# Kernel optimization log

Measured on AMD Instinct MI355X. Metric: run time of the kernel, lower is better.

The kernel has to match this reference:

```python
import jax, jax.numpy as jnp
import numpy as np

B, S, D, DQKV = 4, 2048, 1024, 1024

def setup_inputs() -> dict:
    key = jax.random.key(0)
    kx, kq, kk, kv = jax.random.split(key, 4)
    scale = 1.0 / np.sqrt(D)
    return {
        "x": jax.random.normal(kx, (B, S, D), dtype=jnp.float32),
        "wq": jax.random.normal(kq, (D, DQKV), dtype=jnp.float32) * scale,
        "wk": jax.random.normal(kk, (D, DQKV), dtype=jnp.float32) * scale,
        "wv": jax.random.normal(kv, (D, DQKV), dtype=jnp.float32) * scale,
    }

def reference(x, wq, wk, wv):
    # QKV projections: [B,S,D] @ [D,Dqkv] -> [B,S,Dqkv]
    q = jnp.einsum('bsd,de->bse', x, wq)
    k = jnp.einsum('bsd,de->bse', x, wk)
    v = jnp.einsum('bsd,de->bse', x, wv)
    # scores: [B,S,S], scaled by sqrt(dim_qkv)
    scores = jnp.einsum('bik,bjk->bij', q, k) / jnp.sqrt(jnp.asarray(DQKV, dtype=x.dtype))
    attn = jax.nn.softmax(scores, axis=-1)
    # output: [B,S,Dqkv]
    return jnp.einsum('bij,bjd->bid', attn, v)
```

## Files before the change

### kernel.cpp

```cpp
#include <hip/hip_runtime.h>
#include <cstdint>
#include <cstddef>

typedef __bf16 bf16;
typedef __bf16 bf16x4 __attribute__((ext_vector_type(4)));
typedef __bf16 bf16x8 __attribute__((ext_vector_type(8)));
typedef float  f32x4  __attribute__((ext_vector_type(4)));

#define BATCH 4
#define SEQ   2048
#define DIM   1024
#define LDP   2112

__device__ __forceinline__ bf16 to_bf16(float f) {
    unsigned u = __builtin_bit_cast(unsigned, f);
    u += 0x7fffu + ((u >> 16) & 1u);
    unsigned short h = (unsigned short)(u >> 16);
    return __builtin_bit_cast(bf16, h);
}

__device__ __forceinline__ void load16_lds(const bf16* g, bf16* l) {
    __builtin_amdgcn_global_load_lds(
        (__attribute__((address_space(1))) void*)(g),
        (__attribute__((address_space(3))) void*)(l),
        16, 0, 0);
}

#define BARRIER() do { asm volatile("" ::: "memory"); \
                       __builtin_amdgcn_s_barrier();  \
                       asm volatile("" ::: "memory"); } while (0)
#define LGKM0()   asm volatile("s_waitcnt lgkmcnt(0)" ::: "memory")
#define VM0()     asm volatile("s_waitcnt vmcnt(0)" ::: "memory")


__device__ __forceinline__ void stage_half(
    const bf16* __restrict__ srcRow0, int ld, int k0, bf16* dstHalfBase)
{
    const int tid  = threadIdx.x;
    const int wave = tid >> 6;
    const int lane = tid & 63;
    const int rg   = lane >> 3;
    const int scoff = ((lane & 7) ^ rg) * 8;
#pragma unroll
    for (int j = 0; j < 2; ++j) {
        const int r = wave * 16 + j * 8;
        load16_lds(srcRow0 + (size_t)(r + rg) * ld + k0 + scoff,
                   dstHalfBase + r * 64);
    }
}

__device__ __forceinline__ void gemm_big_core(
    const bf16* __restrict__ Ablk, const bf16* __restrict__ Bblk,
    int K, int lda, int ldb, bf16* As, bf16* Bs, f32x4 acc[8][4])
{
    const int tid  = threadIdx.x;
    const int lane = tid & 63;
    const int wave = tid >> 6;
    const int wr   = wave >> 2;
    const int wc   = wave & 3;
    const int r16  = lane & 15;
    const int g    = lane >> 4;
    const int r7   = r16 & 7;
    const int pk0  = ((g) ^ r7) * 8;
    const int pk1  = ((4 + g) ^ r7) * 8;
    const int arow = (wr * 128 + r16) * 64;
    const int brow = (wc * 64 + r16) * 64;
    const int NT   = K >> 6;

    stage_half(Bblk, ldb, 0, Bs);
    stage_half(Bblk + (size_t)128 * ldb, ldb, 0, Bs + 8192);
    stage_half(Ablk, lda, 0, As);
    stage_half(Ablk + (size_t)128 * lda, lda, 0, As + 8192);
    VM0();
    BARRIER();

#pragma unroll 2
    for (int t = 0; t < NT; ++t) {
        bf16* Ac = As + (t & 1) * 16384;
        bf16* Bc = Bs + (t & 1) * 16384;
        bf16* An = As + ((t + 1) & 1) * 16384;
        bf16* Bn = Bs + ((t + 1) & 1) * 16384;
        const int k1 = (t + 1) << 6;

        bf16x8 b[4][2], a[4][2], a2[4][2];
#pragma unroll
        for (int n = 0; n < 4; ++n) {
            b[n][0] = *(const bf16x8*)(Bc + brow + n * 1024 + pk0);
            b[n][1] = *(const bf16x8*)(Bc + brow + n * 1024 + pk1);
        }
#pragma unroll
        for (int m = 0; m < 4; ++m) {
            a[m][0] = *(const bf16x8*)(Ac + arow + m * 1024 + pk0);
            a[m][1] = *(const bf16x8*)(Ac + arow + m * 1024 + pk1);
        }
        if (t + 1 < NT) {
            stage_half(Bblk, ldb, k1, Bn);
            stage_half(Bblk + (size_t)128 * ldb, ldb, k1, Bn + 8192);
            stage_half(Ablk, lda, k1, An);
            stage_half(Ablk + (size_t)128 * lda, lda, k1, An + 8192);
        }
#pragma unroll
        for (int m = 0; m < 4; ++m)
#pragma unroll
            for (int n = 0; n < 4; ++n)
#pragma unroll
                for (int ks = 0; ks < 2; ++ks)
                    acc[m][n] = __builtin_amdgcn_mfma_f32_16x16x32_bf16(
                        a[m][ks], b[n][ks], acc[m][n], 0, 0, 0);
#pragma unroll
        for (int m = 0; m < 4; ++m) {
            a2[m][0] = *(const bf16x8*)(Ac + arow + 4096 + m * 1024 + pk0);
            a2[m][1] = *(const bf16x8*)(Ac + arow + 4096 + m * 1024 + pk1);
        }
#pragma unroll
        for (int m = 0; m < 4; ++m)
#pragma unroll
            for (int n = 0; n < 4; ++n)
#pragma unroll
                for (int ks = 0; ks < 2; ++ks)
                    acc[4 + m][n] = __builtin_amdgcn_mfma_f32_16x16x32_bf16(
                        a2[m][ks], b[n][ks], acc[4 + m][n], 0, 0, 0);

        LGKM0();
        if (t + 1 < NT) VM0();
        BARRIER();
    }
}

__device__ __forceinline__ void gemm_big_core_n128(
    const bf16* __restrict__ Ablk, const bf16* __restrict__ Bblk,
    int K, int lda, int ldb, bf16* As, bf16* Bs, f32x4 acc[4][4])
{
    const int tid  = threadIdx.x;
    const int lane = tid & 63;
    const int wave = tid >> 6;
    const int wr   = wave >> 1;
    const int wc   = wave & 1;
    const int r16  = lane & 15;
    const int g    = lane >> 4;
    const int r7   = r16 & 7;
    const int pk0  = ((g) ^ r7) * 8;
    const int pk1  = ((4 + g) ^ r7) * 8;
    const int arow = (wr * 64 + r16) * 64;
    const int brow = (wc * 64 + r16) * 64;
    const int NT   = K >> 6;

    stage_half(Ablk, lda, 0, As);
    stage_half(Ablk + (size_t)128 * lda, lda, 0, As + 8192);
    stage_half(Bblk, ldb, 0, Bs);
    VM0();
    BARRIER();

#pragma unroll 2
    for (int t = 0; t < NT; ++t) {
        bf16* Ac = As + (t & 1) * 16384;
        bf16* Bc = Bs + (t & 1) * 8192;
        bf16* An = As + ((t + 1) & 1) * 16384;
        bf16* Bn = Bs + ((t + 1) & 1) * 8192;
        const int k1 = (t + 1) << 6;

        bf16x8 a[4][2], b[4][2];
#pragma unroll
        for (int n = 0; n < 4; ++n) {
            b[n][0] = *(const bf16x8*)(Bc + brow + n * 1024 + pk0);
            b[n][1] = *(const bf16x8*)(Bc + brow + n * 1024 + pk1);
        }
#pragma unroll
        for (int m = 0; m < 4; ++m) {
            a[m][0] = *(const bf16x8*)(Ac + arow + m * 1024 + pk0);
            a[m][1] = *(const bf16x8*)(Ac + arow + m * 1024 + pk1);
        }
        if (t + 1 < NT) {
            stage_half(Ablk, lda, k1, An);
            stage_half(Ablk + (size_t)128 * lda, lda, k1, An + 8192);
            stage_half(Bblk, ldb, k1, Bn);
        }
#pragma unroll
        for (int m = 0; m < 4; ++m)
#pragma unroll
            for (int n = 0; n < 4; ++n)
#pragma unroll
                for (int ks = 0; ks < 2; ++ks)
                    acc[m][n] = __builtin_amdgcn_mfma_f32_16x16x32_bf16(
                        a[m][ks], b[n][ks], acc[m][n], 0, 0, 0);

        LGKM0();
        if (t + 1 < NT) VM0();
        BARRIER();
    }
}

__device__ __forceinline__ void write_c256(
    bf16* __restrict__ Cb, int ldc, const f32x4 acc[8][4])
{
    const int lane = threadIdx.x & 63;
    const int wave = threadIdx.x >> 6;
    const int wr = wave >> 2, wc = wave & 3;
    const int r16 = lane & 15, g = lane >> 4;
    const int row0 = wr * 128 + g * 4;
    const int col0 = wc * 64 + r16;
#pragma unroll
    for (int m = 0; m < 8; ++m)
#pragma unroll
        for (int n = 0; n < 4; ++n)
#pragma unroll
            for (int rr = 0; rr < 4; ++rr)
                Cb[(size_t)(row0 + m * 16 + rr) * ldc + col0 + n * 16] =
                    to_bf16(acc[m][n][rr]);
}

__device__ __forceinline__ void write_c128n(
    bf16* __restrict__ Cb, int ldc, const f32x4 acc[4][4])
{
    const int lane = threadIdx.x & 63;
    const int wave = threadIdx.x >> 6;
    const int wr = wave >> 1, wc = wave & 1;
    const int r16 = lane & 15, g = lane >> 4;
    const int row0 = wr * 64 + g * 4;
    const int col0 = wc * 64 + r16;
#pragma unroll
    for (int m = 0; m < 4; ++m)
#pragma unroll
        for (int n = 0; n < 4; ++n)
#pragma unroll
            for (int rr = 0; rr < 4; ++rr)
                Cb[(size_t)(row0 + m * 16 + rr) * ldc + col0 + n * 16] =
                    to_bf16(acc[m][n][rr]);
}

__global__ __launch_bounds__(512, 2) void proj_qk(
    const bf16* __restrict__ xb, const bf16* __restrict__ Wt,
    bf16* __restrict__ Q, bf16* __restrict__ Kb)
{
    __shared__ bf16 As[32768];
    __shared__ bf16 Bs[32768];
    f32x4 acc[8][4] = {};

    const int p = blockIdx.x;
    const int x = p & 7, s = p >> 3;
    const int my = x * 4 + (s >> 3);
    const int j  = s & 7;
    const bf16* Ab = xb + (size_t)my * 256 * DIM;
    const bf16* Bb = Wt + (size_t)((j >> 2) ? DIM * DIM : 0)
                        + (size_t)(j & 3) * 256 * DIM;
    bf16* dst = (j >> 2) ? Kb : Q;
    bf16* Cb = dst + (size_t)my * 256 * DIM + (size_t)(j & 3) * 256;

    gemm_big_core(Ab, Bb, DIM, DIM, DIM, As, Bs, acc);
    write_c256(Cb, DIM, acc);
}

__global__ __launch_bounds__(512, 2) void proj_v(
    const bf16* __restrict__ xb, const bf16* __restrict__ Wt,
    bf16* __restrict__ Vt)
{
    __shared__ bf16 As[32768];
    __shared__ bf16 Bs[16384];
    f32x4 acc[4][4] = {};

    const int p = blockIdx.x;
    const int x = p & 7, s = p >> 3;
    const int bz = x & 3;
    const int vy = s >> 3;
    const int vx = (x >> 2) * 8 + (s & 7);
    const bf16* Ab = Wt + (size_t)2 * DIM * DIM + (size_t)vy * 256 * DIM;
    const bf16* Bb = xb + (size_t)bz * SEQ * DIM + (size_t)vx * 128 * DIM;
    bf16* Cb = Vt + (size_t)bz * DIM * LDP + (size_t)vy * 256 * LDP
                  + (size_t)vx * 128;

    gemm_big_core_n128(Ab, Bb, DIM, DIM, DIM, As, Bs, acc);
    write_c128n(Cb, LDP, acc);
}

__global__ __launch_bounds__(512, 2) void gemm_scores8(
    const bf16* __restrict__ Qm, const bf16* __restrict__ Kb,
    bf16* __restrict__ P, float* __restrict__ lsum)
{
    __shared__ bf16 As[32768];
    __shared__ bf16 Bs[32768];
    f32x4 acc[8][4] = {};

    const int p = blockIdx.x;
    const int x = p & 7, s = p >> 3;
    const int bz = x & 3;
    const int by = (x >> 2) * 4 + (s >> 3);
    const int bx = s & 7;
    const bf16* Ab = Qm + (size_t)bz * SEQ * DIM + (size_t)by * 256 * DIM;
    const bf16* Bb = Kb + (size_t)bz * SEQ * DIM + (size_t)bx * 256 * DIM;
    gemm_big_core(Ab, Bb, DIM, DIM, DIM, As, Bs, acc);

    bf16* Cb  = P + (size_t)bz * SEQ * LDP;
    float* ls = lsum + (size_t)bz * SEQ;
    const int lane = threadIdx.x & 63;
    const int wave = threadIdx.x >> 6;
    const int wr = wave >> 2, wc = wave & 3;
    const int r16 = lane & 15, g = lane >> 4;
    const int rowB = by * 256 + wr * 128 + g * 4;
    const int colB = bx * 256 + wc * 64 + r16;
#pragma unroll
    for (int m = 0; m < 8; ++m)
#pragma unroll
        for (int rr = 0; rr < 4; ++rr) {
            float sum = 0.0f;
#pragma unroll
            for (int n = 0; n < 4; ++n) {
                const float e = __expf(acc[m][n][rr] * 0.03125f);
                sum += e;
                Cb[(size_t)(rowB + m * 16 + rr) * LDP + colB + n * 16] = to_bf16(e);
            }
            sum += __shfl_xor(sum, 1);
            sum += __shfl_xor(sum, 2);
            sum += __shfl_xor(sum, 4);
            sum += __shfl_xor(sum, 8);
            if (r16 == 0)
                atomicAdd(ls + rowB + m * 16 + rr, sum);
        }
}

__global__ __launch_bounds__(512, 2) void gemm_pv8(
    const bf16* __restrict__ P, const bf16* __restrict__ Vt,
    float* __restrict__ C, const float* __restrict__ lsum)
{
    __shared__ bf16 As[32768];
    __shared__ bf16 Bs[16384];
    f32x4 acc[4][4] = {};

    const int p = blockIdx.x;
    const int x = p & 7, s = p >> 3;
    const int bz = x & 3;
    const int by = (x >> 2) * 4 + (s >> 3);
    const int bx = s & 7;
    const bf16* Ab = P  + (size_t)bz * SEQ * LDP + (size_t)by * 256 * LDP;
    const bf16* Bb = Vt + (size_t)bz * DIM * LDP + (size_t)bx * 128 * LDP;
    gemm_big_core_n128(Ab, Bb, SEQ, LDP, LDP, As, Bs, acc);

    float* Cb = C + (size_t)bz * SEQ * DIM;
    const float* ls = lsum + (size_t)bz * SEQ;
    const int lane = threadIdx.x & 63;
    const int wave = threadIdx.x >> 6;
    const int wr = wave >> 1, wc = wave & 1;
    const int r16 = lane & 15, g = lane >> 4;
    const int row0 = by * 256 + wr * 64 + g * 4;
    const int col0 = bx * 128 + wc * 64 + r16;
#pragma unroll
    for (int m = 0; m < 4; ++m)
#pragma unroll
        for (int rr = 0; rr < 4; ++rr) {
            const int row = row0 + m * 16 + rr;
            const float inv = __builtin_amdgcn_rcpf(ls[row]);
#pragma unroll
            for (int n = 0; n < 4; ++n)
                Cb[(size_t)row * DIM + col0 + n * 16] = acc[m][n][rr] * inv;
        }
}

__global__ __launch_bounds__(256) void prep(
    const float* __restrict__ x,  const float* __restrict__ wq,
    const float* __restrict__ wk, const float* __restrict__ wv,
    bf16* __restrict__ xb, bf16* __restrict__ Wt, float* __restrict__ lsum)
{
    __shared__ float tile[32][33];
    const int b = blockIdx.x;
    const int tid = threadIdx.x;
    if (b < 8192) {
        const size_t i = ((size_t)b * 256 + tid) * 4;
        const float4 v = *(const float4*)(x + i);
        bf16x4 o = { to_bf16(v.x), to_bf16(v.y), to_bf16(v.z), to_bf16(v.w) };
        *(bf16x4*)(xb + i) = o;
    } else if (b < 8192 + 3072) {
        const int t   = b - 8192;
        const int sel = t >> 10;
        const int n0  = (t & 31) * 32;
        const int k0  = ((t >> 5) & 31) * 32;
        const float* w = (sel == 0) ? wq : (sel == 1) ? wk : wv;
        const int tx = tid & 31, ty = tid >> 5;
#pragma unroll
        for (int j = 0; j < 32; j += 8)
            tile[ty + j][tx] = w[(size_t)(k0 + ty + j) * 1024 + n0 + tx];
        __syncthreads();
        bf16* dst = Wt + (size_t)sel * 1024 * 1024;
#pragma unroll
        for (int j = 0; j < 32; j += 8)
            dst[(size_t)(n0 + ty + j) * 1024 + k0 + tx] = to_bf16(tile[tx][ty + j]);
    } else {
#pragma unroll
        for (int i = 0; i < 32; ++i)
            lsum[i * 256 + tid] = 0.0f;
    }
}

extern "C" void kernel_launch(void* const* d_in, const int* in_sizes, int n_in,
                              void* d_out, int out_size, void* d_ws, size_t ws_size,
                              hipStream_t stream)
{
    const float* x  = (const float*)d_in[0];
    const float* wq = (const float*)d_in[1];
    const float* wk = (const float*)d_in[2];
    const float* wv = (const float*)d_in[3];
    float* out = (float*)d_out;
    char* ws = (char*)d_ws;

    bf16*  xb   = (bf16*)(ws);
    bf16*  Wt   = (bf16*)(ws + (16u << 20));
    bf16*  Q    = (bf16*)(ws + (22u << 20));
    bf16*  Kb   = (bf16*)(ws + (38u << 20));
    bf16*  Vt   = (bf16*)(ws + (54u << 20));
    bf16*  P    = (bf16*)(ws + (72u << 20));
    float* lsum = (float*)(ws + (108u << 20));

    prep<<<dim3(8192 + 3072 + 1), dim3(256), 0, stream>>>(
        x, wq, wk, wv, xb, Wt, lsum);

    proj_qk<<<dim3(256), dim3(512), 0, stream>>>(xb, Wt, Q, Kb);
    proj_v<<<dim3(256), dim3(512), 0, stream>>>(xb, Wt, Vt);

    gemm_scores8<<<dim3(256), dim3(512), 0, stream>>>(Q, Kb, P, lsum);

    gemm_pv8<<<dim3(256), dim3(512), 0, stream>>>(P, Vt, out, lsum);
}
```

Measured before the change: 225.8 us.

## Use smaller 128x128 tiles with K=32 staging for V projection and PV GEMMs

Replaces the 256x128 tile, K=64 double-buffered GEMM core used by proj_v and the P·V kernel with a 128x128 tile, K=32 core on 256-thread blocks, using a new swizzled staging routine. Grids grow from 256 to 512 blocks and LDS per block drops sharply, which should raise occupancy and give better wave balance across the CUs. The cost is less operand reuse per tile, more global/L2 traffic, and a barrier every 32-wide K step.

```diff
diff --git a/kernel.cpp b/kernel.cpp
--- a/kernel.cpp
+++ b/kernel.cpp
@@ -127,7 +127,18 @@
     }
 }
 
-__device__ __forceinline__ void gemm_big_core_n128(
+
+__device__ __forceinline__ void stage_q32(
+    const bf16* __restrict__ srcRow0, int ld, int k0, bf16* dstBase)
+{
+    const int t  = threadIdx.x;
+    const int rl = t >> 2;
+    const int c  = (t & 3) ^ ((rl >> 1) & 3);
+    load16_lds(srcRow0 + (size_t)rl * ld + k0 + c * 8,
+               dstBase + (t >> 6) * 512);
+}
+
+__device__ __forceinline__ void gemm_sm_core(
     const bf16* __restrict__ Ablk, const bf16* __restrict__ Bblk,
     int K, int lda, int ldb, bf16* As, bf16* Bs, f32x4 acc[4][4])
 {
@@ -138,51 +149,45 @@
     const int wc   = wave & 1;
     const int r16  = lane & 15;
     const int g    = lane >> 4;
-    const int r7   = r16 & 7;
-    const int pk0  = ((g) ^ r7) * 8;
-    const int pk1  = ((4 + g) ^ r7) * 8;
-    const int arow = (wr * 64 + r16) * 64;
-    const int brow = (wc * 64 + r16) * 64;
-    const int NT   = K >> 6;
-
-    stage_half(Ablk, lda, 0, As);
-    stage_half(Ablk + (size_t)128 * lda, lda, 0, As + 8192);
-    stage_half(Bblk, ldb, 0, Bs);
+    const int pk   = (g ^ ((r16 >> 1) & 3)) * 8;
+    const int arow = (wr * 64 + r16) * 32;
+    const int brow = (wc * 64 + r16) * 32;
+    const int NT   = K >> 5;
+
+    stage_q32(Ablk, lda, 0, As);
+    stage_q32(Ablk + (size_t)64 * lda, lda, 0, As + 2048);
+    stage_q32(Bblk, ldb, 0, Bs);
+    stage_q32(Bblk + (size_t)64 * ldb, ldb, 0, Bs + 2048);
     VM0();
     BARRIER();
 
 #pragma unroll 2
     for (int t = 0; t < NT; ++t) {
-        bf16* Ac = As + (t & 1) * 16384;
-        bf16* Bc = Bs + (t & 1) * 8192;
-        bf16* An = As + ((t + 1) & 1) * 16384;
-        bf16* Bn = Bs + ((t + 1) & 1) * 8192;
-        const int k1 = (t + 1) << 6;
-
-        bf16x8 a[4][2], b[4][2];
-#pragma unroll
-        for (int n = 0; n < 4; ++n) {
-            b[n][0] = *(const bf16x8*)(Bc + brow + n * 1024 + pk0);
-            b[n][1] = *(const bf16x8*)(Bc + brow + n * 1024 + pk1);
-        }
-#pragma unroll
-        for (int m = 0; m < 4; ++m) {
-            a[m][0] = *(const bf16x8*)(Ac + arow + m * 1024 + pk0);
-            a[m][1] = *(const bf16x8*)(Ac + arow + m * 1024 + pk1);
-        }
+        bf16* Ac = As + (t & 1) * 4096;
+        bf16* Bc = Bs + (t & 1) * 4096;
+        bf16* An = As + ((t + 1) & 1) * 4096;
+        bf16* Bn = Bs + ((t + 1) & 1) * 4096;
+        const int k1 = (t + 1) << 5;
+
+        bf16x8 a[4], b[4];
+#pragma unroll
+        for (int n = 0; n < 4; ++n)
+            b[n] = *(const bf16x8*)(Bc + brow + n * 512 + pk);
+#pragma unroll
+        for (int m = 0; m < 4; ++m)
+            a[m] = *(const bf16x8*)(Ac + arow + m * 512 + pk);
         if (t + 1 < NT) {
-            stage_half(Ablk, lda, k1, An);
-            stage_half(Ablk + (size_t)128 * lda, lda, k1, An + 8192);
-            stage_half(Bblk, ldb, k1, Bn);
+            stage_q32(Ablk, lda, k1, An);
+            stage_q32(Ablk + (size_t)64 * lda, lda, k1, An + 2048);
+            stage_q32(Bblk, ldb, k1, Bn);
+            stage_q32(Bblk + (size_t)64 * ldb, ldb, k1, Bn + 2048);
         }
 #pragma unroll
         for (int m = 0; m < 4; ++m)
 #pragma unroll
             for (int n = 0; n < 4; ++n)
-#pragma unroll
-                for (int ks = 0; ks < 2; ++ks)
-                    acc[m][n] = __builtin_amdgcn_mfma_f32_16x16x32_bf16(
-                        a[m][ks], b[n][ks], acc[m][n], 0, 0, 0);
+                acc[m][n] = __builtin_amdgcn_mfma_f32_16x16x32_bf16(
+                    a[m], b[n], acc[m][n], 0, 0, 0);
 
         LGKM0();
         if (t + 1 < NT) VM0();
@@ -201,25 +206,6 @@
     const int col0 = wc * 64 + r16;
 #pragma unroll
     for (int m = 0; m < 8; ++m)
-#pragma unroll
-        for (int n = 0; n < 4; ++n)
-#pragma unroll
-            for (int rr = 0; rr < 4; ++rr)
-                Cb[(size_t)(row0 + m * 16 + rr) * ldc + col0 + n * 16] =
-                    to_bf16(acc[m][n][rr]);
-}
-
-__device__ __forceinline__ void write_c128n(
-    bf16* __restrict__ Cb, int ldc, const f32x4 acc[4][4])
-{
-    const int lane = threadIdx.x & 63;
-    const int wave = threadIdx.x >> 6;
-    const int wr = wave >> 1, wc = wave & 1;
-    const int r16 = lane & 15, g = lane >> 4;
-    const int row0 = wr * 64 + g * 4;
-    const int col0 = wc * 64 + r16;
-#pragma unroll
-    for (int m = 0; m < 4; ++m)
 #pragma unroll
         for (int n = 0; n < 4; ++n)
 #pragma unroll
@@ -250,26 +236,40 @@
     write_c256(Cb, DIM, acc);
 }
 
-__global__ __launch_bounds__(512, 2) void proj_v(
+__global__ __launch_bounds__(256, 2) void proj_v(
     const bf16* __restrict__ xb, const bf16* __restrict__ Wt,
     bf16* __restrict__ Vt)
 {
-    __shared__ bf16 As[32768];
-    __shared__ bf16 Bs[16384];
+    __shared__ bf16 As[8192];
+    __shared__ bf16 Bs[8192];
     f32x4 acc[4][4] = {};
 
     const int p = blockIdx.x;
     const int x = p & 7, s = p >> 3;
     const int bz = x & 3;
+    const int vx = (x >> 2) * 8 + (s & 7);
     const int vy = s >> 3;
-    const int vx = (x >> 2) * 8 + (s & 7);
-    const bf16* Ab = Wt + (size_t)2 * DIM * DIM + (size_t)vy * 256 * DIM;
+    const bf16* Ab = Wt + (size_t)2 * DIM * DIM + (size_t)vy * 128 * DIM;
     const bf16* Bb = xb + (size_t)bz * SEQ * DIM + (size_t)vx * 128 * DIM;
-    bf16* Cb = Vt + (size_t)bz * DIM * LDP + (size_t)vy * 256 * LDP
+    bf16* Cb = Vt + (size_t)bz * DIM * LDP + (size_t)vy * 128 * LDP
                   + (size_t)vx * 128;
 
-    gemm_big_core_n128(Ab, Bb, DIM, DIM, DIM, As, Bs, acc);
-    write_c128n(Cb, LDP, acc);
+    gemm_sm_core(Ab, Bb, DIM, DIM, DIM, As, Bs, acc);
+
+    const int lane = threadIdx.x & 63;
+    const int wave = threadIdx.x >> 6;
+    const int wr = wave >> 1, wc = wave & 1;
+    const int r16 = lane & 15, g = lane >> 4;
+    const int row0 = wr * 64 + g * 4;
+    const int col0 = wc * 64 + r16;
+#pragma unroll
+    for (int m = 0; m < 4; ++m)
+#pragma unroll
+        for (int n = 0; n < 4; ++n)
+#pragma unroll
+            for (int rr = 0; rr < 4; ++rr)
+                Cb[(size_t)(row0 + m * 16 + rr) * LDP + col0 + n * 16] =
+                    to_bf16(acc[m][n][rr]);
 }
 
 __global__ __launch_bounds__(512, 2) void gemm_scores8(
@@ -317,22 +317,22 @@
         }
 }
 
-__global__ __launch_bounds__(512, 2) void gemm_pv8(
+__global__ __launch_bounds__(256, 2) void gemm_pv_sm(
     const bf16* __restrict__ P, const bf16* __restrict__ Vt,
     float* __restrict__ C, const float* __restrict__ lsum)
 {
-    __shared__ bf16 As[32768];
-    __shared__ bf16 Bs[16384];
+    __shared__ bf16 As[8192];
+    __shared__ bf16 Bs[8192];
     f32x4 acc[4][4] = {};
 
     const int p = blockIdx.x;
     const int x = p & 7, s = p >> 3;
     const int bz = x & 3;
-    const int by = (x >> 2) * 4 + (s >> 3);
+    const int by = (x >> 2) * 8 + (s >> 3);
     const int bx = s & 7;
-    const bf16* Ab = P  + (size_t)bz * SEQ * LDP + (size_t)by * 256 * LDP;
+    const bf16* Ab = P  + (size_t)bz * SEQ * LDP + (size_t)by * 128 * LDP;
     const bf16* Bb = Vt + (size_t)bz * DIM * LDP + (size_t)bx * 128 * LDP;
-    gemm_big_core_n128(Ab, Bb, SEQ, LDP, LDP, As, Bs, acc);
+    gemm_sm_core(Ab, Bb, SEQ, LDP, LDP, As, Bs, acc);
 
     float* Cb = C + (size_t)bz * SEQ * DIM;
     const float* ls = lsum + (size_t)bz * SEQ;
@@ -340,7 +340,7 @@
     const int wave = threadIdx.x >> 6;
     const int wr = wave >> 1, wc = wave & 1;
     const int r16 = lane & 15, g = lane >> 4;
-    const int row0 = by * 256 + wr * 64 + g * 4;
+    const int row0 = by * 128 + wr * 64 + g * 4;
     const int col0 = bx * 128 + wc * 64 + r16;
 #pragma unroll
     for (int m = 0; m < 4; ++m)
@@ -412,9 +412,9 @@
         x, wq, wk, wv, xb, Wt, lsum);
 
     proj_qk<<<dim3(256), dim3(512), 0, stream>>>(xb, Wt, Q, Kb);
-    proj_v<<<dim3(256), dim3(512), 0, stream>>>(xb, Wt, Vt);
+    proj_v<<<dim3(512), dim3(256), 0, stream>>>(xb, Wt, Vt);
 
     gemm_scores8<<<dim3(256), dim3(512), 0, stream>>>(Q, Kb, P, lsum);
 
-    gemm_pv8<<<dim3(256), dim3(512), 0, stream>>>(P, Vt, out, lsum);
-}
+    gemm_pv_sm<<<dim3(512), dim3(256), 0, stream>>>(P, Vt, out, lsum);
+}
```

After: 235.2 us. 1.04x slower.
